# Optimization experiments

Hardware: AMD Instinct MI355X
Metric: run time of the kernel (lower is better)

The kernel has to match this reference:

```python
import jax, jax.numpy as jnp
import numpy as np

EPS = 1e-8


def _lstm_cell(xx, h, c, Wih, Whh, bih, bhh):
    g = xx @ Wih.T + bih + h @ Whh.T + bhh
    i, f, gg, o = jnp.split(g, 4, axis=-1)
    i = jax.nn.sigmoid(i); f = jax.nn.sigmoid(f); o = jax.nn.sigmoid(o)
    c2 = f * c + i * jnp.tanh(gg)
    return o * jnp.tanh(c2), c2


def _layernorm(t):
    mu = t.mean(-1, keepdims=True)
    var = t.var(-1, keepdims=True)
    return (t - mu) / jnp.sqrt(var + 1e-5)


def _dnc_forward(x, memory0, Wy, WE, Wr, lstm_params):
    bs, T, xd = x.shape
    N, W = memory0.shape[1], memory0.shape[2]
    R = Wr.shape[0] // W
    hdim = lstm_params[0][1].shape[2]
    L = len(lstm_params)

    def step(carry, x_t):
        M, lrw, u, lww, lrv, h, c = carry
        # BatchNorm1d (training-mode batch stats, affine=identity)
        bn = (x_t - x_t.mean(0)) / jnp.sqrt(x_t.var(0) + 1e-5)
        layer_in = jnp.concatenate([bn, lrv.reshape(bs, W * R)], axis=1)
        # bidirectional multi-layer LSTM, single timestep
        hs, cs = [], []
        for l in range(L):
            Wih, Whh, bih, bhh = lstm_params[l]
            hf, cf = _lstm_cell(layer_in, h[2 * l], c[2 * l], Wih[0], Whh[0], bih[0], bhh[0])
            hb, cb = _lstm_cell(layer_in, h[2 * l + 1], c[2 * l + 1], Wih[1], Whh[1], bih[1], bhh[1])
            layer_in = jnp.concatenate([hf, hb], axis=1)
            hs += [hf, hb]; cs += [cf, cb]
        h_new = jnp.stack(hs); c_new = jnp.stack(cs)  # (2L, bs, h)
        flat = jnp.transpose(h_new, (1, 0, 2)).reshape(bs, 2 * L * hdim)
        vt = flat @ Wy
        iv = _layernorm(flat @ WE)
        # interface parsing (E_t = W*R + 3W + 3R + 3)
        i0 = W * R
        rkeys = iv[:, :i0].reshape(bs, W, R)
        rbeta = 1.0 - jax.nn.log_sigmoid(iv[:, i0:i0 + R]); i0 += R
        wkey = iv[:, i0:i0 + W]; i0 += W
        wbeta = 1.0 - jax.nn.log_sigmoid(iv[:, i0:i0 + 1]); i0 += 1
        erase = jax.nn.sigmoid(iv[:, i0:i0 + W]); i0 += W
        wvec = iv[:, i0:i0 + W]; i0 += W
        fgates = jax.nn.sigmoid(iv[:, i0:i0 + R]); i0 += R
        ag = jax.nn.sigmoid(iv[:, i0:i0 + 1]); i0 += 1
        wg = jax.nn.sigmoid(iv[:, i0:i0 + 1]); i0 += 1
        # read_modes: softmax over a singleton dim -> all ones (content-only read)
        # memory retention and usage
        retention = jnp.prod(1.0 - fgates[:, None, :] * lrw, axis=2)  # (bs, N)
        u_new = (u + lww - u * lww) * retention
        # allocation weighting (sort ascending usage, exclusive cumprod)
        idx = jnp.argsort(u_new, axis=1)
        su = jnp.take_along_axis(u_new, idx, axis=1)
        cp = jnp.cumprod(su, axis=1)
        cp = jnp.concatenate([jnp.ones((bs, 1), su.dtype), cp[:, :-1]], axis=1)
        a_sorted = (1.0 - su) * cp
        alloc = jnp.take_along_axis(a_sorted, jnp.argsort(idx, axis=1), axis=1)
        # write weighting: content + allocation
        Mn = M / (jnp.linalg.norm(M, axis=2, keepdims=True) + EPS)
        kn = wkey / (jnp.linalg.norm(wkey, axis=1, keepdims=True) + EPS)
        cw = jax.nn.softmax(wbeta * jnp.einsum('bnw,bw->bn', Mn, kn), axis=1)
        ww = wg * (ag * alloc + (1.0 - ag) * cw)  # (bs, N)
        # write to memory
        M_new = M * (1.0 - ww[:, :, None] * erase[:, None, :]) + ww[:, :, None] * wvec[:, None, :]
        # content read weightings against updated memory
        Mn2 = M_new / (jnp.linalg.norm(M_new, axis=2, keepdims=True) + EPS)
        rkn = rkeys / (jnp.linalg.norm(rkeys, axis=1, keepdims=True) + EPS)
        sim = jnp.einsum('bnw,bwr->bnr', Mn2, rkn)
        rw = jax.nn.softmax(rbeta[:, None, :] * sim, axis=1)  # (bs, N, R)
        rv = jnp.einsum('bnw,bnr->bwr', M_new, rw)            # (bs, W, R)
        yt = vt + rv.reshape(bs, W * R) @ Wr
        return (M_new, rw, u_new, ww, rv, h_new, c_new), yt

    z = lambda *s: jnp.zeros(s, x.dtype)
    init = (memory0, z(bs, N, R), z(bs, N), z(bs, N), z(bs, W, R),
            z(2 * L, bs, hdim), z(2 * L, bs, hdim))
    _, yts = jax.lax.scan(step, init, jnp.transpose(x, (1, 0, 2)))
    return jnp.max(yts, axis=0)  # max over timesteps, (bs, v_t)


def setup_inputs() -> dict:
    key = jax.random.key(0)
    ks = jax.random.split(key, 16)
    bs, T, xd = 32, 32, 128
    hdim, L, v_t, W, R, N = 512, 2, 2048, 64, 4, 1024
    E_t = W * R + 3 * W + 3 * R + 3  # 463
    u = lambda k, shape, s: jax.random.uniform(k, shape, jnp.float32, -s, s)
    in0, in1 = xd + R * W, 2 * hdim
    sh = 1.0 / np.sqrt(hdim)
    inp = {
        'x': jax.random.normal(ks[0], (bs, T, xd), jnp.float32),
        'memory0': u(ks[1], (bs, N, W), 1.0 / np.sqrt(W)),
        'Wy': u(ks[2], (2 * L * hdim, v_t), 1.0 / np.sqrt(v_t)),
        'WE': u(ks[3], (2 * L * hdim, E_t), 1.0 / np.sqrt(E_t)),
        'Wr': u(ks[4], (W * R, v_t), 1.0 / np.sqrt(v_t)),
        'Wih0': u(ks[5], (2, 4 * hdim, in0), sh),
        'Whh0': u(ks[6], (2, 4 * hdim, hdim), sh),
        'bih0': u(ks[7], (2, 4 * hdim), sh),
        'bhh0': u(ks[8], (2, 4 * hdim), sh),
        'Wih1': u(ks[9], (2, 4 * hdim, in1), sh),
        'Whh1': u(ks[10], (2, 4 * hdim, hdim), sh),
        'bih1': u(ks[11], (2, 4 * hdim), sh),
        'bhh1': u(ks[12], (2, 4 * hdim), sh),
    }
    return inp


def reference(x, memory0, Wy, WE, Wr, Wih0, Whh0, bih0, bhh0, Wih1, Whh1, bih1, bhh1):
    lstm_params = [(Wih0, Whh0, bih0, bhh0), (Wih1, Whh1, bih1, bhh1)]
    return _dnc_forward(x, memory0, Wy, WE, Wr, lstm_params)
```

## Files before the change

kernel.cpp:

```cpp
#include <hip/hip_runtime.h>
#include <math.h>

#define BSZ 32
#define TT  32
#define XD  128
#define HD  512
#define VT  2048
#define ET  463
#define GKS 8
#define VKS 16

__device__ __forceinline__ float sigf(float x){ return 1.f/(1.f+expf(-x)); }
__device__ __forceinline__ float logsigf(float x){
    return (x >= 0.f) ? -log1pf(expf(-x)) : x - log1pf(expf(x));
}

__device__ __forceinline__ float bsum(float v, float* red, int tid){
    #pragma unroll
    for (int off = 32; off > 0; off >>= 1) v += __shfl_xor(v, off);
    if ((tid & 63) == 0) red[tid >> 6] = v;
    __syncthreads();
    if (tid == 0){
        float s = red[0];
        #pragma unroll
        for (int i = 1; i < 16; ++i) s += red[i];
        red[16] = s;
    }
    __syncthreads();
    float r = red[16];
    __syncthreads();
    return r;
}
__device__ __forceinline__ float bmax(float v, float* red, int tid){
    #pragma unroll
    for (int off = 32; off > 0; off >>= 1) v = fmaxf(v, __shfl_xor(v, off));
    if ((tid & 63) == 0) red[tid >> 6] = v;
    __syncthreads();
    if (tid == 0){
        float s = red[0];
        #pragma unroll
        for (int i = 1; i < 16; ++i) s = fmaxf(s, red[i]);
        red[16] = s;
    }
    __syncthreads();
    float r = red[16];
    __syncthreads();
    return r;
}

__global__ void dnc_bnx(const float* __restrict__ x, float* __restrict__ bnx){
    int t = blockIdx.x, k = threadIdx.x;
    float vals[BSZ];
    float s = 0.f;
    #pragma unroll
    for (int b = 0; b < BSZ; ++b){ vals[b] = x[(b*TT + t)*XD + k]; s += vals[b]; }
    float mean = s * (1.f/BSZ);
    float ss = 0.f;
    #pragma unroll
    for (int b = 0; b < BSZ; ++b){ float d = vals[b]-mean; ss += d*d; }
    float inv = 1.f / sqrtf(ss*(1.f/BSZ) + 1e-5f);
    #pragma unroll
    for (int b = 0; b < BSZ; ++b) bnx[((size_t)t*BSZ + b)*XD + k] = (vals[b]-mean)*inv;
}

__global__ __launch_bounds__(256) void dnc_lstm_gemm(
    const float* __restrict__ srcA, int KA,
    const float* __restrict__ srcB, int KB,
    const float* __restrict__ hbase,
    const float* __restrict__ Wih, const float* __restrict__ Whh,
    float* __restrict__ gpart)
{
    const int jc = blockIdx.x, d = blockIdx.y, ks = blockIdx.z;
    const int tid = threadIdx.x;
    const int jg = tid & 31, bg = tid >> 5;
    const int jbase = jc*128;
    const int j0 = jbase + jg*4;
    const int jg4 = jg*4;
    const int b0 = bg*4;
    const int K1 = KA + KB;
    const int cA = KA >> 6;
    const int cin = K1 >> 6;
    const int nct = cin + 8;
    const int per = (nct + GKS - 1) / GKS;
    int c0 = ks*per; int c1 = min(nct, c0+per);
    __shared__ __align__(16) float itile[64*36];
    __shared__ __align__(16) float wtile[64*132];
    float acc[4][4] = {{0}};
    for (int c = c0; c < c1; ++c){
        const float* src; int stride, kb, wcol; const float* Wb; int Kw;
        if (c < cA){ src = srcA; stride = KA; kb = c*64; wcol = c*64;
                     Wb = Wih + (size_t)d*2048*K1; Kw = K1; }
        else if (c < cin){ src = srcB; stride = KB; kb = (c-cA)*64; wcol = c*64;
                           Wb = Wih + (size_t)d*2048*K1; Kw = K1; }
        else { src = hbase + d*(BSZ*HD); stride = HD; kb = (c-cin)*64; wcol = kb;
               Wb = Whh + (size_t)d*2048*512; Kw = 512; }
        #pragma unroll
        for (int i = 0; i < 8; ++i){
            int idx = i*256 + tid; int kk = idx & 63, b = idx >> 6;
            itile[kk*36 + b] = src[b*stride + kb + kk];
        }
        #pragma unroll
        for (int i = 0; i < 8; ++i){
            int fi = i*256 + tid;
            int j  = fi & 127;
            int kq = fi >> 7;
            float4 w4 = *(const float4*)&Wb[(size_t)(jbase + j)*Kw + wcol + kq*4];
            wtile[(kq*4+0)*132 + j] = w4.x;
            wtile[(kq*4+1)*132 + j] = w4.y;
            wtile[(kq*4+2)*132 + j] = w4.z;
            wtile[(kq*4+3)*132 + j] = w4.w;
        }
        __syncthreads();
        #pragma unroll 8
        for (int kk = 0; kk < 64; ++kk){
            float4 a = *(const float4*)&itile[kk*36 + b0];
            float4 w = *(const float4*)&wtile[kk*132 + jg4];
            acc[0][0] += w.x*a.x; acc[0][1] += w.x*a.y; acc[0][2] += w.x*a.z; acc[0][3] += w.x*a.w;
            acc[1][0] += w.y*a.x; acc[1][1] += w.y*a.y; acc[1][2] += w.y*a.z; acc[1][3] += w.y*a.w;
            acc[2][0] += w.z*a.x; acc[2][1] += w.z*a.y; acc[2][2] += w.z*a.z; acc[2][3] += w.z*a.w;
            acc[3][0] += w.w*a.x; acc[3][1] += w.w*a.y; acc[3][2] += w.w*a.z; acc[3][3] += w.w*a.w;
        }
        __syncthreads();
    }
    #pragma unroll
    for (int jj = 0; jj < 4; ++jj){
        #pragma unroll
        for (int bb = 0; bb < 4; ++bb)
            gpart[((size_t)(d*GKS + ks)*BSZ + (b0+bb))*2048 + (j0+jj)] = acc[jj][bb];
    }
}

__global__ void dnc_gates(const float* __restrict__ gpart,
                          const float* __restrict__ bih, const float* __restrict__ bhh,
                          float* __restrict__ cstate, float* __restrict__ hwrite,
                          float* __restrict__ flat, float* __restrict__ lout, int l){
    int idx = blockIdx.x*256 + threadIdx.x;
    int u = idx & 511, b = (idx >> 9) & 31, d = idx >> 14;
    int cell = 2*l + d;
    float g[4];
    #pragma unroll
    for (int xg = 0; xg < 4; ++xg){
        int j = xg*512 + u;
        float s = bih[d*2048 + j] + bhh[d*2048 + j];
        #pragma unroll
        for (int ks = 0; ks < GKS; ++ks)
            s += gpart[((size_t)(d*GKS + ks)*BSZ + b)*2048 + j];
        g[xg] = s;
    }
    float ig = sigf(g[0]), fg = sigf(g[1]), og = sigf(g[3]);
    float gg = tanhf(g[2]);
    int ci = (cell*BSZ + b)*HD + u;
    float c2 = fg*cstate[ci] + ig*gg;
    cstate[ci] = c2;
    float h = og*tanhf(c2);
    hwrite[ci] = h;
    flat[b*2048 + cell*HD + u] = h;
    if (lout) lout[b*1024 + d*HD + u] = h;
}

__global__ void dnc_gemv2(const float* __restrict__ fin, const float* __restrict__ Wy,
                          const float* __restrict__ WE,
                          float* __restrict__ vtp, float* __restrict__ ep){
    const int bx = blockIdx.x, ksi = blockIdx.y;
    const int tid = threadIdx.x;
    const int lane = tid & 63, bg = tid >> 6;
    const int b0 = bg*8;
    const int k0 = ksi*128;
    __shared__ __align__(16) float tile[128*36];
    #pragma unroll
    for (int i = 0; i < 16; ++i){
        int idx = i*256 + tid; int kk = idx & 127, b = idx >> 7;
        tile[kk*36 + b] = fin[b*2048 + k0 + kk];
    }
    __syncthreads();

    if (bx < 8){
        const int m = bx*256 + lane*4;
        float acc[8][4] = {{0}};
        #pragma unroll 4
        for (int kk = 0; kk < 128; ++kk){
            float4 w  = *(const float4*)&Wy[(size_t)(k0+kk)*VT + m];
            float4 a0 = *(const float4*)&tile[kk*36 + b0];
            float4 a1 = *(const float4*)&tile[kk*36 + b0 + 4];
            acc[0][0]+=a0.x*w.x; acc[0][1]+=a0.x*w.y; acc[0][2]+=a0.x*w.z; acc[0][3]+=a0.x*w.w;
            acc[1][0]+=a0.y*w.x; acc[1][1]+=a0.y*w.y; acc[1][2]+=a0.y*w.z; acc[1][3]+=a0.y*w.w;
            acc[2][0]+=a0.z*w.x; acc[2][1]+=a0.z*w.y; acc[2][2]+=a0.z*w.z; acc[2][3]+=a0.z*w.w;
            acc[3][0]+=a0.w*w.x; acc[3][1]+=a0.w*w.y; acc[3][2]+=a0.w*w.z; acc[3][3]+=a0.w*w.w;
            acc[4][0]+=a1.x*w.x; acc[4][1]+=a1.x*w.y; acc[4][2]+=a1.x*w.z; acc[4][3]+=a1.x*w.w;
            acc[5][0]+=a1.y*w.x; acc[5][1]+=a1.y*w.y; acc[5][2]+=a1.y*w.z; acc[5][3]+=a1.y*w.w;
            acc[6][0]+=a1.z*w.x; acc[6][1]+=a1.z*w.y; acc[6][2]+=a1.z*w.z; acc[6][3]+=a1.z*w.w;
            acc[7][0]+=a1.w*w.x; acc[7][1]+=a1.w*w.y; acc[7][2]+=a1.w*w.z; acc[7][3]+=a1.w*w.w;
        }
        #pragma unroll
        for (int bb = 0; bb < 8; ++bb){
            float4 st = make_float4(acc[bb][0], acc[bb][1], acc[bb][2], acc[bb][3]);
            *(float4*)&vtp[((size_t)ksi*BSZ + b0+bb)*VT + m] = st;
        }
    } else {
        const int mb = bx - 8;
        const int m0 = mb*128 + lane, m1 = m0 + 64;
        bool v0 = m0 < ET, v1 = m1 < ET;
        float acc[16] = {0};
        #pragma unroll 2
        for (int kk = 0; kk < 128; ++kk){
            float4 pq = *(const float4*)&tile[kk*36 + b0];
            float4 qq = *(const float4*)&tile[kk*36 + b0 + 4];
            const float* wr = WE + (size_t)(k0+kk)*ET;
            float w0 = v0 ? wr[m0] : 0.f;
            float w1 = v1 ? wr[m1] : 0.f;
            acc[0]+=pq.x*w0; acc[1]+=pq.y*w0; acc[2]+=pq.z*w0; acc[3]+=pq.w*w0;
            acc[4]+=qq.x*w0; acc[5]+=qq.y*w0; acc[6]+=qq.z*w0; acc[7]+=qq.w*w0;
            acc[8]+=pq.x*w1; acc[9]+=pq.y*w1; acc[10]+=pq.z*w1; acc[11]+=pq.w*w1;
            acc[12]+=qq.x*w1; acc[13]+=qq.y*w1; acc[14]+=qq.z*w1; acc[15]+=qq.w*w1;
        }
        if (v0){
            #pragma unroll
            for (int bb = 0; bb < 8; ++bb)
                ep[((size_t)ksi*BSZ + b0+bb)*ET + m0] = acc[bb];
        }
        if (v1){
            #pragma unroll
            for (int bb = 0; bb < 8; ++bb)
                ep[((size_t)ksi*BSZ + b0+bb)*ET + m1] = acc[8+bb];
        }
    }
}

__global__ __launch_bounds__(1024) void dnc_presort_cw(
    const float* __restrict__ ep, const float* __restrict__ lrw,
    const float* __restrict__ lww, float* __restrict__ ubuf,
    float* __restrict__ iv, float* __restrict__ allocw,
    const float* __restrict__ M, float* __restrict__ scw)
{
    const int bid = blockIdx.x, tid = threadIdx.x;
    const int lane = tid & 63, wid = tid >> 6;
    __shared__ float red[32];
    __shared__ float ivS[464];
    __shared__ unsigned long long keysS[1024];
    __shared__ float wtot[16], wpref[16];

    if (bid < 32){
        const int b = bid;
        float myv = 0.f;
        if (tid < ET){
            #pragma unroll
            for (int s = 0; s < VKS; ++s) myv += ep[((size_t)s*BSZ + b)*ET + tid];
        }
        float mean = bsum(myv, red, tid) * (1.f/ET);
        float dd = (tid < ET) ? (myv - mean) : 0.f;
        float var = bsum(dd*dd, red, tid) * (1.f/ET);
        float rinv = 1.f / sqrtf(var + 1e-5f);
        float ivv = (myv - mean)*rinv;
        if (tid < ET){ ivS[tid] = ivv; iv[b*ET + tid] = ivv; }
        __syncthreads();

        const int n = tid;
        float4 lw4 = *(const float4*)&lrw[((size_t)b*1024 + n)*4];
        float f0 = sigf(ivS[453]), f1 = sigf(ivS[454]), f2 = sigf(ivS[455]), f3 = sigf(ivS[456]);
        float ret = (1.f-f0*lw4.x)*(1.f-f1*lw4.y)*(1.f-f2*lw4.z)*(1.f-f3*lw4.w);
        float uo = ubuf[b*1024+n], lwo = lww[b*1024+n];
        float un = (uo + lwo - uo*lwo)*ret;
        ubuf[b*1024+n] = un;

        unsigned long long key = ((unsigned long long)__float_as_uint(un) << 32) | (unsigned)tid;
        for (int k = 2; k <= 1024; k <<= 1){
            int j = k >> 1;
            for (; j >= 64; j >>= 1){
                keysS[tid] = key; __syncthreads();
                unsigned long long other = keysS[tid ^ j];
                bool up = ((tid & k) == 0);
                bool takeMin = (((tid & j) == 0) == up);
                key = takeMin ? (key < other ? key : other) : (key > other ? key : other);
                __syncthreads();
            }
            for (; j >= 1; j >>= 1){
                unsigned long long other = __shfl_xor(key, j);
                bool up = ((tid & k) == 0);
                bool takeMin = (((tid & j) == 0) == up);
                key = takeMin ? (key < other ? key : other) : (key > other ? key : other);
            }
        }
        float su = __uint_as_float((unsigned)(key >> 32));
        int idxv = (int)(key & 0xffffffffu);

        float p = su;
        #pragma unroll
        for (int o = 1; o < 64; o <<= 1){ float q = __shfl_up(p, o); if (lane >= o) p *= q; }
        if (lane == 63) wtot[wid] = p;
        __syncthreads();
        if (tid == 0){
            float r = 1.f;
            #pragma unroll
            for (int i = 0; i < 16; ++i){ wpref[i] = r; r *= wtot[i]; }
        }
        __syncthreads();
        float excl = __shfl_up(p, 1); if (lane == 0) excl = 1.f;
        float cpx = excl * wpref[wid];
        allocw[b*1024 + idxv] = (1.f - su)*cpx;
    } else {
        const int b = bid - 32;
        float myv = 0.f;
        if (tid < ET){
            #pragma unroll
            for (int s = 0; s < VKS; ++s) myv += ep[((size_t)s*BSZ + b)*ET + tid];
        }
        float mean = bsum(myv, red, tid) * (1.f/ET);
        float dd = (tid < ET) ? (myv - mean) : 0.f;
        float var = bsum(dd*dd, red, tid) * (1.f/ET);
        float rinv = 1.f / sqrtf(var + 1e-5f);
        float ivv = (myv - mean)*rinv;
        if (tid >= 260 && tid < 324) ivS[tid - 260] = ivv;
        if (tid == 324) ivS[64] = 1.f - logsigf(ivv);
        __syncthreads();
        float ksq = 0.f;
        #pragma unroll
        for (int w = 0; w < 64; ++w) ksq += ivS[w]*ivS[w];
        float kden = sqrtf(ksq) + 1e-8f;
        float wb = ivS[64];
        const float* Mrow = M + ((size_t)b*1024 + tid)*64;
        float dot = 0.f, msq = 0.f;
        #pragma unroll
        for (int w = 0; w < 64; w += 4){
            float4 mv = *(const float4*)(Mrow + w);
            dot += mv.x*ivS[w] + mv.y*ivS[w+1] + mv.z*ivS[w+2] + mv.w*ivS[w+3];
            msq += mv.x*mv.x + mv.y*mv.y + mv.z*mv.z + mv.w*mv.w;
        }
        scw[b*1024 + tid] = wb*dot/((sqrtf(msq) + 1e-8f)*kden);
    }
}

__global__ __launch_bounds__(1024) void dnc_memup_rv(
    float* __restrict__ M, const float* __restrict__ scw,
    const float* __restrict__ allocw, const float* __restrict__ iv,
    float* __restrict__ lww, float* __restrict__ lrw, float* __restrict__ lrv)
{
    const int b = blockIdx.x, tid = threadIdx.x;
    const int lane = tid & 63, wid = tid >> 6;
    __shared__ float red[32];
    __shared__ float aux[400];
    __shared__ float pS[4096];
    __shared__ float rvS[1024];
    const int n = tid;

    float s = scw[b*1024 + n];
    float mx = bmax(s, red, tid);
    float tot = bsum(expf(s - mx), red, tid);
    float cwv = expf(s - mx)/tot;
    float ag = sigf(iv[b*ET + 457]), wg = sigf(iv[b*ET + 458]);
    float wwv = wg*(ag*allocw[b*1024 + n] + (1.f-ag)*cwv);
    lww[b*1024 + n] = wwv;

    if (tid < 64){ aux[tid] = sigf(iv[b*ET + 325 + tid]); aux[64+tid] = iv[b*ET + 389 + tid]; }
    if (tid >= 64 && tid < 320) aux[64 + tid] = iv[b*ET + (tid - 64)];
    if (tid >= 320 && tid < 324) aux[72 + tid] = 1.f - logsigf(iv[b*ET + 256 + (tid - 320)]);
    __syncthreads();
    if (tid < 4){
        float ss = 0.f;
        #pragma unroll
        for (int w = 0; w < 64; ++w){ float v = aux[128 + w*4 + tid]; ss += v*v; }
        aux[384 + tid] = sqrtf(ss) + 1e-8f;
    }
    __syncthreads();
    if (tid < 256) aux[128 + tid] = aux[128 + tid] / aux[384 + (tid & 3)];
    __syncthreads();

    float* Mrow = M + ((size_t)b*1024 + n)*64;
    float dr0=0.f, dr1=0.f, dr2=0.f, dr3=0.f, msq2=0.f;
    #pragma unroll
    for (int w = 0; w < 64; w += 4){
        float4 mv = *(const float4*)(Mrow + w);
        mv.x = mv.x*(1.f - wwv*aux[w+0]) + wwv*aux[64+w+0];
        mv.y = mv.y*(1.f - wwv*aux[w+1]) + wwv*aux[64+w+1];
        mv.z = mv.z*(1.f - wwv*aux[w+2]) + wwv*aux[64+w+2];
        mv.w = mv.w*(1.f - wwv*aux[w+3]) + wwv*aux[64+w+3];
        *(float4*)(Mrow + w) = mv;
        msq2 += mv.x*mv.x + mv.y*mv.y + mv.z*mv.z + mv.w*mv.w;
        dr0 += mv.x*aux[128+(w+0)*4+0] + mv.y*aux[128+(w+1)*4+0] + mv.z*aux[128+(w+2)*4+0] + mv.w*aux[128+(w+3)*4+0];
        dr1 += mv.x*aux[128+(w+0)*4+1] + mv.y*aux[128+(w+1)*4+1] + mv.z*aux[128+(w+2)*4+1] + mv.w*aux[128+(w+3)*4+1];
        dr2 += mv.x*aux[128+(w+0)*4+2] + mv.y*aux[128+(w+1)*4+2] + mv.z*aux[128+(w+2)*4+2] + mv.w*aux[128+(w+3)*4+2];
        dr3 += mv.x*aux[128+(w+0)*4+3] + mv.y*aux[128+(w+1)*4+3] + mv.z*aux[128+(w+2)*4+3] + mv.w*aux[128+(w+3)*4+3];
    }
    float den = sqrtf(msq2) + 1e-8f;
    pS[0*1024 + n] = aux[392]*dr0/den;
    pS[1*1024 + n] = aux[393]*dr1/den;
    pS[2*1024 + n] = aux[394]*dr2/den;
    pS[3*1024 + n] = aux[395]*dr3/den;
    __syncthreads();

    const int r_ = tid >> 8, i4 = (tid & 255)*4;
    float v0 = pS[r_*1024 + i4+0], v1 = pS[r_*1024 + i4+1];
    float v2 = pS[r_*1024 + i4+2], v3 = pS[r_*1024 + i4+3];
    float lm = fmaxf(fmaxf(v0,v1), fmaxf(v2,v3));
    #pragma unroll
    for (int off = 32; off > 0; off >>= 1) lm = fmaxf(lm, __shfl_xor(lm, off));
    if (lane == 0) red[wid] = lm;
    __syncthreads();
    if (tid < 4) red[16+tid] = fmaxf(fmaxf(red[4*tid],red[4*tid+1]), fmaxf(red[4*tid+2],red[4*tid+3]));
    __syncthreads();
    float mxr = red[16 + r_];
    float lsum = expf(v0-mxr) + expf(v1-mxr) + expf(v2-mxr) + expf(v3-mxr);
    #pragma unroll
    for (int off = 32; off > 0; off >>= 1) lsum += __shfl_xor(lsum, off);
    if (lane == 0) red[wid] = lsum;
    __syncthreads();
    if (tid < 4) red[20+tid] = red[4*tid]+red[4*tid+1]+red[4*tid+2]+red[4*tid+3];
    __syncthreads();
    float totr = red[20 + r_];
    {
        float w0 = expf(v0-mxr)/totr, w1 = expf(v1-mxr)/totr;
        float w2 = expf(v2-mxr)/totr, w3 = expf(v3-mxr)/totr;
        pS[r_*1024 + i4+0] = w0; pS[r_*1024 + i4+1] = w1;
        pS[r_*1024 + i4+2] = w2; pS[r_*1024 + i4+3] = w3;
        lrw[((size_t)(b*1024 + i4+0))*4 + r_] = w0;
        lrw[((size_t)(b*1024 + i4+1))*4 + r_] = w1;
        lrw[((size_t)(b*1024 + i4+2))*4 + r_] = w2;
        lrw[((size_t)(b*1024 + i4+3))*4 + r_] = w3;
    }
    __syncthreads();

    {
        const int q = tid >> 8, r = (tid >> 6) & 3, w = tid & 63;
        const float* Mb = M + ((size_t)b*1024 + q*256)*64;
        const float* rb = pS + r*1024 + q*256;
        float acc = 0.f;
        for (int i = 0; i < 256; ++i)
            acc += Mb[(size_t)i*64 + w] * rb[i];
        rvS[tid] = acc;
    }
    __syncthreads();
    if (tid < 256){
        int w2 = tid >> 2, r2 = tid & 3;
        float ssum = 0.f;
        #pragma unroll
        for (int q = 0; q < 4; ++q) ssum += rvS[q*256 + r2*64 + w2];
        lrv[b*256 + tid] = ssum;
    }
}

__global__ void dnc_yfin(const float* __restrict__ lrv, const float* __restrict__ Wr,
                         const float* __restrict__ vtp, float* __restrict__ out, int t){
    const int tid = threadIdx.x;
    const int mg = tid & 31, bgl = tid >> 5;
    const int m0 = blockIdx.x*128 + mg*4;
    const int b  = blockIdx.y*8 + bgl;
    __shared__ float lt[256*9];
    #pragma unroll
    for (int i = 0; i < 8; ++i)
        lt[tid*9 + i] = lrv[((size_t)(blockIdx.y*8 + i))*256 + tid];
    __syncthreads();
    float4 acc = make_float4(0.f,0.f,0.f,0.f);
    for (int kk = 0; kk < 256; ++kk){
        float av = lt[kk*9 + bgl];
        float4 wv = *(const float4*)&Wr[(size_t)kk*VT + m0];
        acc.x += av*wv.x; acc.y += av*wv.y; acc.z += av*wv.z; acc.w += av*wv.w;
    }
    #pragma unroll
    for (int sp = 0; sp < VKS; ++sp){
        float4 vp = *(const float4*)&vtp[((size_t)sp*BSZ + b)*VT + m0];
        acc.x += vp.x; acc.y += vp.y; acc.z += vp.z; acc.w += vp.w;
    }
    float4* op = (float4*)&out[(size_t)b*VT + m0];
    if (t == 0){ *op = acc; }
    else {
        float4 cur = *op;
        cur.x = fmaxf(cur.x, acc.x); cur.y = fmaxf(cur.y, acc.y);
        cur.z = fmaxf(cur.z, acc.z); cur.w = fmaxf(cur.w, acc.w);
        *op = cur;
    }
}

extern "C" void kernel_launch(void* const* d_in, const int* in_sizes, int n_in,
                              void* d_out, int out_size, void* d_ws, size_t ws_size,
                              hipStream_t stream){
    const float* x      = (const float*)d_in[0];
    const float* mem0   = (const float*)d_in[1];
    const float* Wy     = (const float*)d_in[2];
    const float* WE     = (const float*)d_in[3];
    const float* Wr     = (const float*)d_in[4];
    const float* Wih0   = (const float*)d_in[5];
    const float* Whh0   = (const float*)d_in[6];
    const float* bih0   = (const float*)d_in[7];
    const float* bhh0   = (const float*)d_in[8];
    const float* Wih1   = (const float*)d_in[9];
    const float* Whh1   = (const float*)d_in[10];
    const float* bih1   = (const float*)d_in[11];
    const float* bhh1   = (const float*)d_in[12];
    float* out = (float*)d_out;

    float* p = (float*)d_ws;
    float* M       = p; p += (size_t)BSZ*1024*64;
    float* hstate0 = p; p += 4*BSZ*HD;
    float* hstate1 = p; p += 4*BSZ*HD;
    float* cstate  = p; p += 4*BSZ*HD;
    float* ubuf    = p; p += BSZ*1024;
    float* lww     = p; p += BSZ*1024;
    float* lrw     = p; p += BSZ*1024*4;
    float* lrv     = p; p += BSZ*256;
    float* bnx     = p; p += (size_t)TT*BSZ*XD;
    float* lin1    = p; p += BSZ*1024;
    float* gpart   = p; p += (size_t)2*GKS*BSZ*2048;
    float* flat    = p; p += BSZ*2048;
    float* vtp     = p; p += (size_t)VKS*BSZ*VT;
    float* ep      = p; p += (size_t)VKS*BSZ*ET;
    float* iv      = p; p += BSZ*ET;
    float* allocw  = p; p += BSZ*1024;
    float* scw     = p; p += BSZ*1024;

    (void)hipMemcpyAsync(M, mem0, (size_t)BSZ*1024*64*sizeof(float), hipMemcpyDeviceToDevice, stream);
    size_t zfloats = (size_t)(4*BSZ*HD)*3 + BSZ*1024*2 + BSZ*1024*4 + BSZ*256;
    (void)hipMemsetAsync(hstate0, 0, zfloats*sizeof(float), stream);

    dnc_bnx<<<TT, 128, 0, stream>>>(x, bnx);

    for (int t = 0; t < TT; ++t){
        const float* hr = (t & 1) ? hstate1 : hstate0;
        float*       hw = (t & 1) ? hstate0 : hstate1;
        dnc_lstm_gemm<<<dim3(16,2,GKS), 256, 0, stream>>>(bnx + (size_t)t*BSZ*XD, XD,
            lrv, 256, hr, Wih0, Whh0, gpart);
        dnc_gates<<<128, 256, 0, stream>>>(gpart, bih0, bhh0, cstate, hw, flat, lin1, 0);
        dnc_lstm_gemm<<<dim3(16,2,GKS), 256, 0, stream>>>(lin1, 1024,
            nullptr, 0, hr + 2*BSZ*HD, Wih1, Whh1, gpart);
        dnc_gates<<<128, 256, 0, stream>>>(gpart, bih1, bhh1, cstate, hw, flat, nullptr, 1);
        dnc_gemv2<<<dim3(12,VKS), 256, 0, stream>>>(flat, Wy, WE, vtp, ep);
        dnc_presort_cw<<<64, 1024, 0, stream>>>(ep, lrw, lww, ubuf, iv, allocw, M, scw);
        dnc_memup_rv<<<32, 1024, 0, stream>>>(M, scw, allocw, iv, lww, lrw, lrv);
        dnc_yfin<<<dim3(16,4), 256, 0, stream>>>(lrv, Wr, vtp, out, t);
    }
}
```

Before: 4.116 ms.

## Fuse previous-step output projection into layer-0 LSTM GEMM and restructure read-vector loop

The output projection (yfin) for step t-1 now runs as extra blocks inside the layer-0 LSTM GEMM launch of step t, with one final yfin launch after the loop. This removes one kernel launch per timestep and lets the small projection overlap with the GEMM. Separately, the read-vector computation in dnc_memup_rv reads the just-written read weights from global as float4 and accumulates all four read heads per thread over 64 rows, instead of staging them in shared memory and looping 256 rows per head. This cuts per-thread serial work and redundant memory-row loads, at the cost of a larger shared reduction buffer and a global write-then-read of lrw within the block.

New measurement: 3.919 ms. -4.8%, faster.

```diff
diff --git a/kernel.cpp b/kernel.cpp
--- a/kernel.cpp
+++ b/kernel.cpp
@@ -63,15 +63,14 @@
     for (int b = 0; b < BSZ; ++b) bnx[((size_t)t*BSZ + b)*XD + k] = (vals[b]-mean)*inv;
 }
 
-__global__ __launch_bounds__(256) void dnc_lstm_gemm(
+__device__ __forceinline__ void lstm_gemm_body(
     const float* __restrict__ srcA, int KA,
     const float* __restrict__ srcB, int KB,
     const float* __restrict__ hbase,
     const float* __restrict__ Wih, const float* __restrict__ Whh,
-    float* __restrict__ gpart)
+    float* __restrict__ gpart, int jc, int d, int ks, int tid,
+    float* itile, float* wtile)
 {
-    const int jc = blockIdx.x, d = blockIdx.y, ks = blockIdx.z;
-    const int tid = threadIdx.x;
     const int jg = tid & 31, bg = tid >> 5;
     const int jbase = jc*128;
     const int j0 = jbase + jg*4;
@@ -83,8 +82,6 @@
     const int nct = cin + 8;
     const int per = (nct + GKS - 1) / GKS;
     int c0 = ks*per; int c1 = min(nct, c0+per);
-    __shared__ __align__(16) float itile[64*36];
-    __shared__ __align__(16) float wtile[64*132];
     float acc[4][4] = {{0}};
     for (int c = c0; c < c1; ++c){
         const float* src; int stride, kb, wcol; const float* Wb; int Kw;
@@ -128,6 +125,79 @@
         for (int bb = 0; bb < 4; ++bb)
             gpart[((size_t)(d*GKS + ks)*BSZ + (b0+bb))*2048 + (j0+jj)] = acc[jj][bb];
     }
+}
+
+__device__ __forceinline__ void yfin_body(
+    const float* __restrict__ lrv, const float* __restrict__ Wr,
+    const float* __restrict__ vtp, float* __restrict__ out, int t,
+    int mi, int bgi, int tid, float* lt)
+{
+    const int mg = tid & 31, bgl = tid >> 5;
+    const int m0 = mi*128 + mg*4;
+    const int b  = bgi*8 + bgl;
+    #pragma unroll
+    for (int i = 0; i < 8; ++i)
+        lt[tid*9 + i] = lrv[((size_t)(bgi*8 + i))*256 + tid];
+    __syncthreads();
+    float4 acc = make_float4(0.f,0.f,0.f,0.f);
+    for (int kk = 0; kk < 256; ++kk){
+        float av = lt[kk*9 + bgl];
+        float4 wv = *(const float4*)&Wr[(size_t)kk*VT + m0];
+        acc.x += av*wv.x; acc.y += av*wv.y; acc.z += av*wv.z; acc.w += av*wv.w;
+    }
+    #pragma unroll
+    for (int sp = 0; sp < VKS; ++sp){
+        float4 vp = *(const float4*)&vtp[((size_t)sp*BSZ + b)*VT + m0];
+        acc.x += vp.x; acc.y += vp.y; acc.z += vp.z; acc.w += vp.w;
+    }
+    float4* op = (float4*)&out[(size_t)b*VT + m0];
+    if (t == 0){ *op = acc; }
+    else {
+        float4 cur = *op;
+        cur.x = fmaxf(cur.x, acc.x); cur.y = fmaxf(cur.y, acc.y);
+        cur.z = fmaxf(cur.z, acc.z); cur.w = fmaxf(cur.w, acc.w);
+        *op = cur;
+    }
+}
+
+__global__ __launch_bounds__(256) void dnc_gemm0_yfin(
+    const float* __restrict__ srcA,
+    const float* __restrict__ lrv, const float* __restrict__ hbase,
+    const float* __restrict__ Wih, const float* __restrict__ Whh,
+    float* __restrict__ gpart,
+    const float* __restrict__ Wr, const float* __restrict__ vtp,
+    float* __restrict__ out, int tprev)
+{
+    __shared__ __align__(16) float itile[64*36];
+    __shared__ __align__(16) float wtile[64*132];
+    const int bid = blockIdx.x, tid = threadIdx.x;
+    if (bid < 256){
+        lstm_gemm_body(srcA, XD, lrv, 256, hbase, Wih, Whh, gpart,
+                       bid & 15, (bid >> 4) & 1, bid >> 5, tid, itile, wtile);
+    } else {
+        if (tprev < 0) return;
+        int yb = bid - 256;
+        yfin_body(lrv, Wr, vtp, out, tprev, yb & 15, yb >> 4, tid, itile);
+    }
+}
+
+__global__ __launch_bounds__(256) void dnc_lstm_gemm(
+    const float* __restrict__ srcA, int KA,
+    const float* __restrict__ srcB, int KB,
+    const float* __restrict__ hbase,
+    const float* __restrict__ Wih, const float* __restrict__ Whh,
+    float* __restrict__ gpart)
+{
+    __shared__ __align__(16) float itile[64*36];
+    __shared__ __align__(16) float wtile[64*132];
+    lstm_gemm_body(srcA, KA, srcB, KB, hbase, Wih, Whh, gpart,
+                   blockIdx.x, blockIdx.y, blockIdx.z, threadIdx.x, itile, wtile);
+}
+
+__global__ void dnc_yfin(const float* __restrict__ lrv, const float* __restrict__ Wr,
+                         const float* __restrict__ vtp, float* __restrict__ out, int t){
+    __shared__ float lt[256*9];
+    yfin_body(lrv, Wr, vtp, out, t, blockIdx.x, blockIdx.y, threadIdx.x, lt);
 }
 
 __global__ void dnc_gates(const float* __restrict__ gpart,
@@ -339,7 +409,7 @@
     __shared__ float red[32];
     __shared__ float aux[400];
     __shared__ float pS[4096];
-    __shared__ float rvS[1024];
+    __shared__ float rvS[4096];
     const int n = tid;
 
     float s = scw[b*1024 + n];
@@ -407,65 +477,37 @@
     __syncthreads();
     float totr = red[20 + r_];
     {
-        float w0 = expf(v0-mxr)/totr, w1 = expf(v1-mxr)/totr;
-        float w2 = expf(v2-mxr)/totr, w3 = expf(v3-mxr)/totr;
-        pS[r_*1024 + i4+0] = w0; pS[r_*1024 + i4+1] = w1;
-        pS[r_*1024 + i4+2] = w2; pS[r_*1024 + i4+3] = w3;
-        lrw[((size_t)(b*1024 + i4+0))*4 + r_] = w0;
-        lrw[((size_t)(b*1024 + i4+1))*4 + r_] = w1;
-        lrw[((size_t)(b*1024 + i4+2))*4 + r_] = w2;
-        lrw[((size_t)(b*1024 + i4+3))*4 + r_] = w3;
+        lrw[((size_t)(b*1024 + i4+0))*4 + r_] = expf(v0-mxr)/totr;
+        lrw[((size_t)(b*1024 + i4+1))*4 + r_] = expf(v1-mxr)/totr;
+        lrw[((size_t)(b*1024 + i4+2))*4 + r_] = expf(v2-mxr)/totr;
+        lrw[((size_t)(b*1024 + i4+3))*4 + r_] = expf(v3-mxr)/totr;
     }
     __syncthreads();
 
     {
-        const int q = tid >> 8, r = (tid >> 6) & 3, w = tid & 63;
-        const float* Mb = M + ((size_t)b*1024 + q*256)*64;
-        const float* rb = pS + r*1024 + q*256;
-        float acc = 0.f;
-        for (int i = 0; i < 256; ++i)
-            acc += Mb[(size_t)i*64 + w] * rb[i];
-        rvS[tid] = acc;
+        const int w = tid & 63, g = tid >> 6;
+        const float* Mb = M + (size_t)b*65536;
+        const float* rwb = lrw + (size_t)b*4096;
+        float a0=0.f, a1=0.f, a2=0.f, a3=0.f;
+        #pragma unroll 4
+        for (int i = 0; i < 64; ++i){
+            int n2 = g*64 + i;
+            float m = Mb[(size_t)n2*64 + w];
+            float4 rw4 = *(const float4*)&rwb[n2*4];
+            a0 += m*rw4.x; a1 += m*rw4.y; a2 += m*rw4.z; a3 += m*rw4.w;
+        }
+        rvS[(0*16 + g)*64 + w] = a0;
+        rvS[(1*16 + g)*64 + w] = a1;
+        rvS[(2*16 + g)*64 + w] = a2;
+        rvS[(3*16 + g)*64 + w] = a3;
     }
     __syncthreads();
     if (tid < 256){
         int w2 = tid >> 2, r2 = tid & 3;
         float ssum = 0.f;
         #pragma unroll
-        for (int q = 0; q < 4; ++q) ssum += rvS[q*256 + r2*64 + w2];
+        for (int g = 0; g < 16; ++g) ssum += rvS[(r2*16 + g)*64 + w2];
         lrv[b*256 + tid] = ssum;
-    }
-}
-
-__global__ void dnc_yfin(const float* __restrict__ lrv, const float* __restrict__ Wr,
-                         const float* __restrict__ vtp, float* __restrict__ out, int t){
-    const int tid = threadIdx.x;
-    const int mg = tid & 31, bgl = tid >> 5;
-    const int m0 = blockIdx.x*128 + mg*4;
-    const int b  = blockIdx.y*8 + bgl;
-    __shared__ float lt[256*9];
-    #pragma unroll
-    for (int i = 0; i < 8; ++i)
-        lt[tid*9 + i] = lrv[((size_t)(blockIdx.y*8 + i))*256 + tid];
-    __syncthreads();
-    float4 acc = make_float4(0.f,0.f,0.f,0.f);
-    for (int kk = 0; kk < 256; ++kk){
-        float av = lt[kk*9 + bgl];
-        float4 wv = *(const float4*)&Wr[(size_t)kk*VT + m0];
-        acc.x += av*wv.x; acc.y += av*wv.y; acc.z += av*wv.z; acc.w += av*wv.w;
-    }
-    #pragma unroll
-    for (int sp = 0; sp < VKS; ++sp){
-        float4 vp = *(const float4*)&vtp[((size_t)sp*BSZ + b)*VT + m0];
-        acc.x += vp.x; acc.y += vp.y; acc.z += vp.z; acc.w += vp.w;
-    }
-    float4* op = (float4*)&out[(size_t)b*VT + m0];
-    if (t == 0){ *op = acc; }
-    else {
-        float4 cur = *op;
-        cur.x = fmaxf(cur.x, acc.x); cur.y = fmaxf(cur.y, acc.y);
-        cur.z = fmaxf(cur.z, acc.z); cur.w = fmaxf(cur.w, acc.w);
-        *op = cur;
     }
 }
 
@@ -515,8 +557,8 @@
     for (int t = 0; t < TT; ++t){
         const float* hr = (t & 1) ? hstate1 : hstate0;
         float*       hw = (t & 1) ? hstate0 : hstate1;
-        dnc_lstm_gemm<<<dim3(16,2,GKS), 256, 0, stream>>>(bnx + (size_t)t*BSZ*XD, XD,
-            lrv, 256, hr, Wih0, Whh0, gpart);
+        dnc_gemm0_yfin<<<320, 256, 0, stream>>>(bnx + (size_t)t*BSZ*XD,
+            lrv, hr, Wih0, Whh0, gpart, Wr, vtp, out, t - 1);
         dnc_gates<<<128, 256, 0, stream>>>(gpart, bih0, bhh0, cstate, hw, flat, lin1, 0);
         dnc_lstm_gemm<<<dim3(16,2,GKS), 256, 0, stream>>>(lin1, 1024,
             nullptr, 0, hr + 2*BSZ*HD, Wih1, Whh1, gpart);
@@ -524,6 +566,6 @@
         dnc_gemv2<<<dim3(12,VKS), 256, 0, stream>>>(flat, Wy, WE, vtp, ep);
         dnc_presort_cw<<<64, 1024, 0, stream>>>(ep, lrw, lww, ubuf, iv, allocw, M, scw);
         dnc_memup_rv<<<32, 1024, 0, stream>>>(M, scw, allocw, iv, lww, lrw, lrv);
-        dnc_yfin<<<dim3(16,4), 256, 0, stream>>>(lrv, Wr, vtp, out, t);
-    }
-}
+    }
+    dnc_yfin<<<dim3(16,4), 256, 0, stream>>>(lrv, Wr, vtp, out, TT - 1);
+}
```
